# Kernel tuning notes

Measured on AMD Instinct MI355X. Metric: run time of the kernel, lower is better.

## Reference

```python
import jax, jax.numpy as jnp
import numpy as np

B, S, D, H = 2, 4096, 768, 12
DH = D // H
SCALE = 1.0 / DH ** 0.5


def setup_inputs() -> dict:
    key = jax.random.key(0)
    k1, k2, k3, k4, k5 = jax.random.split(key, 5)
    x = jax.random.normal(k1, (B, S, D), dtype=jnp.float32)
    # nn.Linear weights: stored as [out, in]; init ~ U(-1/sqrt(in), 1/sqrt(in))
    lim = 1.0 / np.sqrt(D)
    W_qkv = jax.random.uniform(k2, (3 * D, D), minval=-lim, maxval=lim, dtype=jnp.float32)
    b_qkv = jax.random.uniform(k3, (3 * D,), minval=-lim, maxval=lim, dtype=jnp.float32)
    W_out = jax.random.uniform(k4, (D, D), minval=-lim, maxval=lim, dtype=jnp.float32)
    b_out = jax.random.uniform(k5, (D,), minval=-lim, maxval=lim, dtype=jnp.float32)
    return {"x": x, "W_qkv": W_qkv, "b_qkv": b_qkv, "W_out": W_out, "b_out": b_out}


def reference(x, W_qkv, b_qkv, W_out, b_out):
    bs, ns, _ = x.shape
    qkv = x @ W_qkv.T + b_qkv                       # [B, S, 3D]
    qkv = qkv.reshape(bs, ns, 3, H, DH)
    qkv = jnp.transpose(qkv, (2, 0, 3, 1, 4))        # [3, B, H, S, DH]
    q, k, v = qkv[0], qkv[1], qkv[2]
    attn = jnp.einsum('bhqd,bhkd->bhqk', q, k)       # [B, H, S, S]
    attn = jax.nn.softmax(attn * SCALE, axis=-1)
    out = jnp.einsum('bhqk,bhkd->bhqd', attn, v)     # [B, H, S, DH]
    out = jnp.transpose(out, (0, 2, 1, 3)).reshape(bs, ns, D)
    return out @ W_out.T + b_out
```

## Files before the change

kernel.cpp:

```cpp
#include <hip/hip_runtime.h>
#include <hip/hip_bf16.h>
#include <stdint.h>

#define B_    2
#define S_    4096
#define D_    768
#define H_    12
#define DH_   64
#define BH_   (B_*H_)
#define M_    (B_*S_)
#define NQKV_ 2304
#define QSCALE_ 0.18033688011112042f

typedef unsigned short bf16u;
typedef short bf16x8 __attribute__((ext_vector_type(8)));
typedef float f32x4 __attribute__((ext_vector_type(4)));

__device__ __forceinline__ bf16u f2bf(float f) {
    unsigned u = __float_as_uint(f);
    u += 0x7FFFu + ((u >> 16) & 1u);
    return (bf16u)(u >> 16);
}

__device__ __forceinline__ unsigned f2bf_pk(float a, float b) {
    return (unsigned)f2bf(a) | ((unsigned)f2bf(b) << 16);
}

__device__ __forceinline__ void gl_lds16(const void* g, void* l) {
    __builtin_amdgcn_global_load_lds(
        (const __attribute__((address_space(1))) unsigned*)g,
        (__attribute__((address_space(3))) unsigned*)l, 16, 0, 0);
}

#define N1Q_ 1572864
#define N2Q_  442368
#define N3Q_  147456
__global__ __launch_bounds__(256) void convert3_kernel(
    const float* __restrict__ s1, const float* __restrict__ s2,
    const float* __restrict__ s3, bf16u* __restrict__ d1,
    bf16u* __restrict__ d2, bf16u* __restrict__ d3)
{
    int i = blockIdx.x * 256 + threadIdx.x;
    const float* s; bf16u* d; int j;
    if (i < N1Q_)              { s = s1; d = d1; j = i; }
    else if (i < N1Q_ + N2Q_)  { s = s2; d = d2; j = i - N1Q_; }
    else                       { s = s3; d = d3; j = i - N1Q_ - N2Q_; }
    float4 v = ((const float4*)s)[j];
    ushort4 o;
    o.x = f2bf(v.x); o.y = f2bf(v.y); o.z = f2bf(v.z); o.w = f2bf(v.w);
    ((ushort4*)d)[j] = o;
}

template<int EPI>
__global__ __launch_bounds__(256) void gemm_kernel(
    const bf16u* __restrict__ A, const bf16u* __restrict__ Bw,
    const float* __restrict__ bias, float* __restrict__ Cout,
    bf16u* __restrict__ Qb, bf16u* __restrict__ Kb, bf16u* __restrict__ Vtb)
{
    __shared__ bf16u As[2][128*32];
    __shared__ bf16u Bs[2][128*32];
    const int tid  = threadIdx.x;
    const int lane = tid & 63;
    const int wave = tid >> 6;
    const int wr = wave >> 1, wc = wave & 1;
    const int lr = lane & 15;
    const int quad = lane >> 4;

    const int nwg  = gridDim.x * gridDim.y;
    const int fblk = blockIdx.y * gridDim.x + blockIdx.x;
    const int vblk = (fblk & 7) * (nwg >> 3) + (fblk >> 3);
    const int m0 = (vblk / gridDim.x) * 128;
    const int n0 = (vblk % gridDim.x) * 128;

    f32x4 acc[4][4];
    #pragma unroll
    for (int i = 0; i < 4; i++)
        #pragma unroll
        for (int j = 0; j < 4; j++)
            acc[i][j] = (f32x4){0.f, 0.f, 0.f, 0.f};

    auto stage = [&](int k0, int bf) {
        #pragma unroll
        for (int r = 0; r < 2; r++) {
            int c = r * 256 + tid;
            int row = c >> 2;
            int col = ((c & 3) ^ (row & 3)) * 8;
            gl_lds16(A  + (size_t)(m0 + row) * 768 + k0 + col,
                     (char*)&As[bf][0] + c * 16);
            gl_lds16(Bw + (size_t)(n0 + row) * 768 + k0 + col,
                     (char*)&Bs[bf][0] + c * 16);
        }
    };

    stage(0, 0);

    auto body = [&](int k0, int buf, bool do_stage) __attribute__((always_inline)) {
        __syncthreads();
        if (do_stage) stage(k0 + 32, buf ^ 1);
        bf16x8 af[4], bg[4];
        #pragma unroll
        for (int t = 0; t < 4; t++) {
            int ra = wr * 64 + t * 16 + lr;
            int rb = wc * 64 + t * 16 + lr;
            af[t] = *(const bf16x8*)(&As[buf][0] + ra * 32 + ((quad ^ (ra & 3)) * 8));
            bg[t] = *(const bf16x8*)(&Bs[buf][0] + rb * 32 + ((quad ^ (rb & 3)) * 8));
        }
        __builtin_amdgcn_s_setprio(1);
        #pragma unroll
        for (int i = 0; i < 4; i++)
            #pragma unroll
            for (int j = 0; j < 4; j++)
                acc[i][j] = __builtin_amdgcn_mfma_f32_16x16x32_bf16(
                    af[i], bg[j], acc[i][j], 0, 0, 0);
        __builtin_amdgcn_s_setprio(0);
    };

    #pragma unroll 1
    for (int k0 = 0; k0 < 768 - 64; k0 += 64) {
        body(k0,      0, true);
        body(k0 + 32, 1, true);
    }
    body(768 - 64, 0, true);
    body(768 - 32, 1, false);

    #pragma unroll
    for (int i = 0; i < 4; i++) {
        int mbase = m0 + wr * 64 + i * 16 + quad * 4;
        #pragma unroll
        for (int j = 0; j < 4; j++) {
            int n = n0 + wc * 64 + j * 16 + lr;
            float bv = bias[n];
            if (EPI == 0) {
                #pragma unroll
                for (int r = 0; r < 4; r++)
                    Cout[(size_t)(mbase + r) * 768 + n] = acc[i][j][r] + bv;
            } else {
                int t3  = n / 768;
                int rem = n - t3 * 768;
                int h   = rem >> 6;
                int dh  = rem & 63;
                int b   = mbase >> 12;
                int s0  = mbase & 4095;
                int bh  = b * H_ + h;
                if (t3 == 2) {
                    uint2 pk;
                    pk.x = f2bf_pk(acc[i][j][0] + bv, acc[i][j][1] + bv);
                    pk.y = f2bf_pk(acc[i][j][2] + bv, acc[i][j][3] + bv);
                    *(uint2*)(Vtb + ((size_t)bh * DH_ + dh) * S_ + s0) = pk;
                } else if (t3 == 0) {
                    #pragma unroll
                    for (int r = 0; r < 4; r++)
                        Qb[((size_t)bh * S_ + s0 + r) * DH_ + dh] =
                            f2bf((acc[i][j][r] + bv) * QSCALE_);
                } else {
                    #pragma unroll
                    for (int r = 0; r < 4; r++)
                        Kb[((size_t)bh * S_ + s0 + r) * DH_ + dh] =
                            f2bf(acc[i][j][r] + bv);
                }
            }
        }
    }
}

__global__ __launch_bounds__(512, 6) void attn_kernel(
    const bf16u* __restrict__ Qb, const bf16u* __restrict__ Kb,
    const bf16u* __restrict__ Vtb, bf16u* __restrict__ A2)
{
    __shared__ char Lds[32768];
    const int tid  = threadIdx.x;
    const int lane = tid & 63;
    const int w    = tid >> 6;
    const int lr   = lane & 15;
    const int quad = lane >> 4;

    const int fblk = blockIdx.y * gridDim.x + blockIdx.x;
    const int vblk = (fblk & 7) * 96 + (fblk >> 3);
    const int q0   = (vblk & 31) * 128;
    const int bh   = vblk >> 5;

    const size_t kbase_g = (size_t)bh * S_ * DH_;
    const size_t vbase_g = (size_t)bh * DH_ * S_;

    bf16x8 aq0, aq1;
    {
        const size_t qb = ((size_t)bh * S_ + q0 + w * 16 + lr) * DH_ + quad * 8;
        aq0 = *(const bf16x8*)(Qb + qb);
        aq1 = *(const bf16x8*)(Qb + qb + 32);
    }

    bf16x8 onesf;
    #pragma unroll
    for (int j = 0; j < 8; j++) onesf[j] = (short)0x3F80;

    f32x4 o[4];
    f32x4 l_acc = (f32x4){0.f, 0.f, 0.f, 0.f};
    #pragma unroll
    for (int t = 0; t < 4; t++) o[t] = (f32x4){0.f, 0.f, 0.f, 0.f};

    int kvaddr[4][2];
    #pragma unroll
    for (int nt = 0; nt < 4; nt++) {
        int rk = nt * 16 + lr;
        kvaddr[nt][0] = (rk * 64 + ((quad ^ (rk & 7)) * 8)) * 2;
        kvaddr[nt][1] = (rk * 64 + (((4 + quad) ^ (rk & 7)) * 8)) * 2;
    }

    auto stage = [&](int kv0, int bf) {
        int c = tid;
        int row = c >> 3;
        int col = ((c & 7) ^ (row & 7)) * 8;
        gl_lds16(Kb  + kbase_g + (size_t)(kv0 + row) * DH_ + col,
                 Lds + bf * 8192 + c * 16);
        gl_lds16(Vtb + vbase_g + (size_t)row * S_ + kv0 + col,
                 Lds + 16384 + bf * 8192 + c * 16);
    };

    stage(0, 0);

    auto body = [&](int it, int buf, bool do_stage) __attribute__((always_inline)) {
        __syncthreads();
        if (do_stage) stage((it + 1) * 64, buf ^ 1);

        const char* Kbuf = Lds + buf * 8192;
        const char* Vbuf = Lds + 16384 + buf * 8192;

        f32x4 sc[4];
        __builtin_amdgcn_s_setprio(1);
        #pragma unroll
        for (int nt = 0; nt < 4; nt++) {
            const bf16x8 bk0 = *(const bf16x8*)(Kbuf + kvaddr[nt][0]);
            const bf16x8 bk1 = *(const bf16x8*)(Kbuf + kvaddr[nt][1]);
            f32x4 s = (f32x4){0.f, 0.f, 0.f, 0.f};
            s = __builtin_amdgcn_mfma_f32_16x16x32_bf16(bk0, aq0, s, 0, 0, 0);
            s = __builtin_amdgcn_mfma_f32_16x16x32_bf16(bk1, aq1, s, 0, 0, 0);
            sc[nt] = s;
        }
        __builtin_amdgcn_s_setprio(0);

        unsigned W[4][2];
        #pragma unroll
        for (int nt = 0; nt < 4; nt++) {
            float p0 = __builtin_amdgcn_exp2f(sc[nt][0]);
            float p1 = __builtin_amdgcn_exp2f(sc[nt][1]);
            float p2 = __builtin_amdgcn_exp2f(sc[nt][2]);
            float p3 = __builtin_amdgcn_exp2f(sc[nt][3]);
            W[nt][0] = __builtin_amdgcn_perm(__float_as_uint(p1),
                                             __float_as_uint(p0), 0x07060302u);
            W[nt][1] = __builtin_amdgcn_perm(__float_as_uint(p3),
                                             __float_as_uint(p2), 0x07060302u);
        }

        bf16x8 ap[2];
        #pragma unroll
        for (int ks = 0; ks < 2; ks++) {
            union { unsigned u[4]; bf16x8 v; } Af;
            #pragma unroll
            for (int b = 0; b < 2; b++) {
                auto r1 = __builtin_amdgcn_permlane32_swap(
                    W[2 * ks][b], W[2 * ks + 1][b], false, false);
                auto r2 = __builtin_amdgcn_permlane16_swap(
                    r1[0], r1[1], false, false);
                Af.u[b]     = r2[0];
                Af.u[2 + b] = r2[1];
            }
            ap[ks] = Af.v;
        }

        __builtin_amdgcn_s_setprio(1);
        l_acc = __builtin_amdgcn_mfma_f32_16x16x32_bf16(ap[0], onesf, l_acc, 0, 0, 0);
        l_acc = __builtin_amdgcn_mfma_f32_16x16x32_bf16(ap[1], onesf, l_acc, 0, 0, 0);
        #pragma unroll
        for (int nt = 0; nt < 4; nt++) {
            const bf16x8 bv0 = *(const bf16x8*)(Vbuf + kvaddr[nt][0]);
            const bf16x8 bv1 = *(const bf16x8*)(Vbuf + kvaddr[nt][1]);
            o[nt] = __builtin_amdgcn_mfma_f32_16x16x32_bf16(ap[0], bv0, o[nt], 0, 0, 0);
            o[nt] = __builtin_amdgcn_mfma_f32_16x16x32_bf16(ap[1], bv1, o[nt], 0, 0, 0);
        }
        __builtin_amdgcn_s_setprio(0);
    };

    #pragma unroll 1
    for (int it = 0; it < S_ / 64 - 2; it += 2) {
        body(it,     0, true);
        body(it + 1, 1, true);
    }
    body(S_ / 64 - 2, 0, true);
    body(S_ / 64 - 1, 1, false);

    const int b = bh / H_, h = bh % H_;
    float rl[4];
    #pragma unroll
    for (int r2 = 0; r2 < 4; r2++) rl[r2] = 1.0f / l_acc[r2];
    #pragma unroll
    for (int nt = 0; nt < 4; nt++)
        #pragma unroll
        for (int r2 = 0; r2 < 4; r2++) {
            int q = q0 + w * 16 + quad * 4 + r2;
            float v = o[nt][r2] * rl[r2];
            A2[((size_t)b * S_ + q) * D_ + h * DH_ + nt * 16 + lr] = f2bf(v);
        }
}

extern "C" void kernel_launch(void* const* d_in, const int* in_sizes, int n_in,
                              void* d_out, int out_size, void* d_ws, size_t ws_size,
                              hipStream_t stream) {
    const float* x     = (const float*)d_in[0];
    const float* W_qkv = (const float*)d_in[1];
    const float* b_qkv = (const float*)d_in[2];
    const float* W_out = (const float*)d_in[3];
    const float* b_out = (const float*)d_in[4];
    float* out = (float*)d_out;
    char* ws = (char*)d_ws;

    bf16u* xb    = (bf16u*)(ws + 0);
    bf16u* wqkvb = (bf16u*)(ws + 12582912);
    bf16u* woutb = (bf16u*)(ws + 16121856);
    bf16u* Qb    = (bf16u*)(ws + 17301504);
    bf16u* Kb    = (bf16u*)(ws + 29884416);
    bf16u* Vtb   = (bf16u*)(ws + 42467328);
    bf16u* A2    = (bf16u*)(ws + 55050240);

    convert3_kernel<<<(N1Q_ + N2Q_ + N3Q_) / 256, 256, 0, stream>>>(
        x, W_qkv, W_out, xb, wqkvb, woutb);

    dim3 g1(NQKV_/128, M_/128);
    gemm_kernel<1><<<g1, 256, 0, stream>>>(xb, wqkvb, b_qkv, nullptr, Qb, Kb, Vtb);

    dim3 g2(S_/128, BH_);
    attn_kernel<<<g2, 512, 0, stream>>>(Qb, Kb, Vtb, A2);

    dim3 g3(D_/128, M_/128);
    gemm_kernel<0><<<g3, 256, 0, stream>>>(A2, woutb, b_out, out, nullptr, nullptr, nullptr);
}
```

Before: 267.6 us.

## Split KV range across two warp groups, 32 query rows per warp, LDS reduction

The attention kernel now splits its 8 warps into two groups that each process half of the key/value sequence. Each warp handles 32 query rows instead of 16, so every K and V fragment read from LDS feeds two MFMAs. The two groups merge their partial output and row-sum accumulators through LDS at the end. This is meant to cut LDS read traffic per MFMA and raise arithmetic intensity. In exchange it doubles accumulator register pressure, adds an epilogue reduction with extra barriers, and changes the V LDS layout and swizzle.

```diff
diff --git a/kernel.cpp b/kernel.cpp
--- a/kernel.cpp
+++ b/kernel.cpp
@@ -167,10 +167,12 @@
     const bf16u* __restrict__ Qb, const bf16u* __restrict__ Kb,
     const bf16u* __restrict__ Vtb, bf16u* __restrict__ A2)
 {
-    __shared__ char Lds[32768];
+    __shared__ char Lds[33280];
     const int tid  = threadIdx.x;
     const int lane = tid & 63;
     const int w    = tid >> 6;
+    const int grp  = w >> 2;
+    const int wq   = (w & 3) * 32;
     const int lr   = lane & 15;
     const int quad = lane >> 4;
 
@@ -182,124 +184,175 @@
     const size_t kbase_g = (size_t)bh * S_ * DH_;
     const size_t vbase_g = (size_t)bh * DH_ * S_;
 
-    bf16x8 aq0, aq1;
-    {
-        const size_t qb = ((size_t)bh * S_ + q0 + w * 16 + lr) * DH_ + quad * 8;
-        aq0 = *(const bf16x8*)(Qb + qb);
-        aq1 = *(const bf16x8*)(Qb + qb + 32);
+    bf16x8 aq[2][2];
+    #pragma unroll
+    for (int rh = 0; rh < 2; rh++) {
+        const size_t qb = ((size_t)bh * S_ + q0 + wq + rh * 16 + lr) * DH_ + quad * 8;
+        aq[rh][0] = *(const bf16x8*)(Qb + qb);
+        aq[rh][1] = *(const bf16x8*)(Qb + qb + 32);
     }
 
     bf16x8 onesf;
     #pragma unroll
     for (int j = 0; j < 8; j++) onesf[j] = (short)0x3F80;
 
-    f32x4 o[4];
-    f32x4 l_acc = (f32x4){0.f, 0.f, 0.f, 0.f};
-    #pragma unroll
-    for (int t = 0; t < 4; t++) o[t] = (f32x4){0.f, 0.f, 0.f, 0.f};
-
-    int kvaddr[4][2];
+    f32x4 o[2][4];
+    f32x4 l_acc[2];
+    #pragma unroll
+    for (int rh = 0; rh < 2; rh++) {
+        l_acc[rh] = (f32x4){0.f, 0.f, 0.f, 0.f};
+        #pragma unroll
+        for (int t = 0; t < 4; t++) o[rh][t] = (f32x4){0.f, 0.f, 0.f, 0.f};
+    }
+
+    int kaddr[2][2];
+    #pragma unroll
+    for (int ntk = 0; ntk < 2; ntk++) {
+        int rk = ntk * 16 + lr;
+        kaddr[ntk][0] = rk * 128 + ((quad ^ (rk & 7)) * 16);
+        kaddr[ntk][1] = rk * 128 + (((4 + quad) ^ (rk & 7)) * 16);
+    }
+    int vaddr[4];
     #pragma unroll
     for (int nt = 0; nt < 4; nt++) {
-        int rk = nt * 16 + lr;
-        kvaddr[nt][0] = (rk * 64 + ((quad ^ (rk & 7)) * 8)) * 2;
-        kvaddr[nt][1] = (rk * 64 + (((4 + quad) ^ (rk & 7)) * 8)) * 2;
-    }
-
-    auto stage = [&](int kv0, int bf) {
-        int c = tid;
-        int row = c >> 3;
-        int col = ((c & 7) ^ (row & 7)) * 8;
-        gl_lds16(Kb  + kbase_g + (size_t)(kv0 + row) * DH_ + col,
-                 Lds + bf * 8192 + c * 16);
-        gl_lds16(Vtb + vbase_g + (size_t)row * S_ + kv0 + col,
-                 Lds + 16384 + bf * 8192 + c * 16);
+        int rv = nt * 16 + lr;
+        int sr = rv >> 1;
+        int slot = ((rv & 1) << 2) | quad;
+        vaddr[nt] = sr * 128 + ((slot ^ (sr & 7)) * 16);
+    }
+
+    auto stage = [&](int u, int pp) {
+        const int g  = tid >> 8;
+        const int c  = tid & 255;
+        const int kv0 = g * (S_ / 2) + u * 32;
+        int krow = c >> 3;
+        int kcol = ((c & 7) ^ (krow & 7)) * 8;
+        gl_lds16(Kb + kbase_g + (size_t)(kv0 + krow) * DH_ + kcol,
+                 Lds + pp * 8192 + g * 4096 + c * 16);
+        int sr = c >> 3;
+        int lslot = (c & 7) ^ (sr & 7);
+        int dh  = sr * 2 + (lslot >> 2);
+        int kvc = (lslot & 3) * 8;
+        gl_lds16(Vtb + vbase_g + (size_t)dh * S_ + kv0 + kvc,
+                 Lds + 16384 + pp * 8192 + g * 4096 + c * 16);
     };
 
     stage(0, 0);
 
-    auto body = [&](int it, int buf, bool do_stage) __attribute__((always_inline)) {
+    auto body = [&](int u, int pp, bool do_stage) __attribute__((always_inline)) {
         __syncthreads();
-        if (do_stage) stage((it + 1) * 64, buf ^ 1);
-
-        const char* Kbuf = Lds + buf * 8192;
-        const char* Vbuf = Lds + 16384 + buf * 8192;
-
-        f32x4 sc[4];
+        if (do_stage) stage(u + 1, pp ^ 1);
+
+        const char* Kbuf = Lds + pp * 8192 + grp * 4096;
+        const char* Vbuf = Lds + 16384 + pp * 8192 + grp * 4096;
+
+        f32x4 sc[2][2];
         __builtin_amdgcn_s_setprio(1);
         #pragma unroll
-        for (int nt = 0; nt < 4; nt++) {
-            const bf16x8 bk0 = *(const bf16x8*)(Kbuf + kvaddr[nt][0]);
-            const bf16x8 bk1 = *(const bf16x8*)(Kbuf + kvaddr[nt][1]);
-            f32x4 s = (f32x4){0.f, 0.f, 0.f, 0.f};
-            s = __builtin_amdgcn_mfma_f32_16x16x32_bf16(bk0, aq0, s, 0, 0, 0);
-            s = __builtin_amdgcn_mfma_f32_16x16x32_bf16(bk1, aq1, s, 0, 0, 0);
-            sc[nt] = s;
+        for (int ntk = 0; ntk < 2; ntk++) {
+            const bf16x8 bk0 = *(const bf16x8*)(Kbuf + kaddr[ntk][0]);
+            const bf16x8 bk1 = *(const bf16x8*)(Kbuf + kaddr[ntk][1]);
+            #pragma unroll
+            for (int rh = 0; rh < 2; rh++) {
+                f32x4 s = (f32x4){0.f, 0.f, 0.f, 0.f};
+                s = __builtin_amdgcn_mfma_f32_16x16x32_bf16(bk0, aq[rh][0], s, 0, 0, 0);
+                s = __builtin_amdgcn_mfma_f32_16x16x32_bf16(bk1, aq[rh][1], s, 0, 0, 0);
+                sc[rh][ntk] = s;
+            }
         }
         __builtin_amdgcn_s_setprio(0);
 
-        unsigned W[4][2];
-        #pragma unroll
-        for (int nt = 0; nt < 4; nt++) {
-            float p0 = __builtin_amdgcn_exp2f(sc[nt][0]);
-            float p1 = __builtin_amdgcn_exp2f(sc[nt][1]);
-            float p2 = __builtin_amdgcn_exp2f(sc[nt][2]);
-            float p3 = __builtin_amdgcn_exp2f(sc[nt][3]);
-            W[nt][0] = __builtin_amdgcn_perm(__float_as_uint(p1),
-                                             __float_as_uint(p0), 0x07060302u);
-            W[nt][1] = __builtin_amdgcn_perm(__float_as_uint(p3),
-                                             __float_as_uint(p2), 0x07060302u);
+        unsigned W[2][2][2];
+        #pragma unroll
+        for (int rh = 0; rh < 2; rh++) {
+            #pragma unroll
+            for (int ntk = 0; ntk < 2; ntk++) {
+                float p0 = __builtin_amdgcn_exp2f(sc[rh][ntk][0]);
+                float p1 = __builtin_amdgcn_exp2f(sc[rh][ntk][1]);
+                float p2 = __builtin_amdgcn_exp2f(sc[rh][ntk][2]);
+                float p3 = __builtin_amdgcn_exp2f(sc[rh][ntk][3]);
+                W[rh][ntk][0] = __builtin_amdgcn_perm(__float_as_uint(p1),
+                                                      __float_as_uint(p0), 0x07060302u);
+                W[rh][ntk][1] = __builtin_amdgcn_perm(__float_as_uint(p3),
+                                                      __float_as_uint(p2), 0x07060302u);
+            }
         }
 
         bf16x8 ap[2];
         #pragma unroll
-        for (int ks = 0; ks < 2; ks++) {
-            union { unsigned u[4]; bf16x8 v; } Af;
+        for (int rh = 0; rh < 2; rh++) {
+            union { unsigned u4[4]; bf16x8 v; } Af;
             #pragma unroll
             for (int b = 0; b < 2; b++) {
                 auto r1 = __builtin_amdgcn_permlane32_swap(
-                    W[2 * ks][b], W[2 * ks + 1][b], false, false);
+                    W[rh][0][b], W[rh][1][b], false, false);
                 auto r2 = __builtin_amdgcn_permlane16_swap(
                     r1[0], r1[1], false, false);
-                Af.u[b]     = r2[0];
-                Af.u[2 + b] = r2[1];
+                Af.u4[b]     = r2[0];
+                Af.u4[2 + b] = r2[1];
             }
-            ap[ks] = Af.v;
+            ap[rh] = Af.v;
         }
 
         __builtin_amdgcn_s_setprio(1);
-        l_acc = __builtin_amdgcn_mfma_f32_16x16x32_bf16(ap[0], onesf, l_acc, 0, 0, 0);
-        l_acc = __builtin_amdgcn_mfma_f32_16x16x32_bf16(ap[1], onesf, l_acc, 0, 0, 0);
+        #pragma unroll
+        for (int rh = 0; rh < 2; rh++)
+            l_acc[rh] = __builtin_amdgcn_mfma_f32_16x16x32_bf16(ap[rh], onesf, l_acc[rh], 0, 0, 0);
         #pragma unroll
         for (int nt = 0; nt < 4; nt++) {
-            const bf16x8 bv0 = *(const bf16x8*)(Vbuf + kvaddr[nt][0]);
-            const bf16x8 bv1 = *(const bf16x8*)(Vbuf + kvaddr[nt][1]);
-            o[nt] = __builtin_amdgcn_mfma_f32_16x16x32_bf16(ap[0], bv0, o[nt], 0, 0, 0);
-            o[nt] = __builtin_amdgcn_mfma_f32_16x16x32_bf16(ap[1], bv1, o[nt], 0, 0, 0);
+            const bf16x8 bv = *(const bf16x8*)(Vbuf + vaddr[nt]);
+            #pragma unroll
+            for (int rh = 0; rh < 2; rh++)
+                o[rh][nt] = __builtin_amdgcn_mfma_f32_16x16x32_bf16(ap[rh], bv, o[rh][nt], 0, 0, 0);
         }
         __builtin_amdgcn_s_setprio(0);
     };
 
     #pragma unroll 1
-    for (int it = 0; it < S_ / 64 - 2; it += 2) {
-        body(it,     0, true);
-        body(it + 1, 1, true);
-    }
-    body(S_ / 64 - 2, 0, true);
-    body(S_ / 64 - 1, 1, false);
-
-    const int b = bh / H_, h = bh % H_;
-    float rl[4];
-    #pragma unroll
-    for (int r2 = 0; r2 < 4; r2++) rl[r2] = 1.0f / l_acc[r2];
-    #pragma unroll
-    for (int nt = 0; nt < 4; nt++)
-        #pragma unroll
-        for (int r2 = 0; r2 < 4; r2++) {
-            int q = q0 + w * 16 + quad * 4 + r2;
-            float v = o[nt][r2] * rl[r2];
-            A2[((size_t)b * S_ + q) * D_ + h * DH_ + nt * 16 + lr] = f2bf(v);
-        }
+    for (int u = 0; u < 62; u += 2) {
+        body(u,     0, true);
+        body(u + 1, 1, true);
+    }
+    body(62, 0, true);
+    body(63, 1, false);
+
+    __syncthreads();
+    float* LO = (float*)Lds;
+    float* LL = (float*)(Lds + 32768);
+    if (grp == 0) {
+        #pragma unroll
+        for (int rh = 0; rh < 2; rh++) {
+            #pragma unroll
+            for (int r2 = 0; r2 < 4; r2++)
+                LL[wq + rh * 16 + quad * 4 + r2] = l_acc[rh][r2];
+            #pragma unroll
+            for (int nt = 0; nt < 4; nt++)
+                #pragma unroll
+                for (int r2 = 0; r2 < 4; r2++)
+                    LO[(wq + rh * 16 + quad * 4 + r2) * 64 + nt * 16 + lr] =
+                        o[rh][nt][r2];
+        }
+    }
+    __syncthreads();
+    if (grp == 1) {
+        const int b = bh / H_, h = bh % H_;
+        #pragma unroll
+        for (int rh = 0; rh < 2; rh++) {
+            float rl[4];
+            #pragma unroll
+            for (int r2 = 0; r2 < 4; r2++)
+                rl[r2] = 1.0f / (l_acc[rh][r2] + LL[wq + rh * 16 + quad * 4 + r2]);
+            #pragma unroll
+            for (int nt = 0; nt < 4; nt++)
+                #pragma unroll
+                for (int r2 = 0; r2 < 4; r2++) {
+                    int row = wq + rh * 16 + quad * 4 + r2;
+                    int q = q0 + row;
+                    float v = (o[rh][nt][r2] + LO[row * 64 + nt * 16 + lr]) * rl[r2];
+                    A2[((size_t)b * S_ + q) * D_ + h * DH_ + nt * 16 + lr] = f2bf(v);
+                }
+        }
+    }
 }
 
 extern "C" void kernel_launch(void* const* d_in, const int* in_sizes, int n_in,
```

After: 685.0 us. 2.56x slower.
